# Optimization experiments

Measured on AMD Instinct MI355X. Metric: run time of the kernel, lower is better.

Reference implementation:

```python
import jax, jax.numpy as jnp
import numpy as np

# Dimensions
B, T_ENC, T_DEC = 64, 128, 64          # batch, encoder frames, max_video_length
DH, DV, CHUNK = 1024, 2048, 8          # dim_hidden, dim_video, ON-LSTM chunk size
NCH = DV // CHUNK                      # number of chunks (256)
G = 4 * DV + 2 * NCH                   # gate width of ON-LSTM cell


def setup_inputs() -> dict:
    key = jax.random.key(0)
    ks = jax.random.split(key, 6)
    s = lambda n: 1.0 / np.sqrt(n)
    return {
        "encoder_outputs": jax.random.normal(ks[0], (B, T_ENC, DH), jnp.float32),
        "encoder_hidden": jnp.zeros((1, B, DH), jnp.float32),  # unused by forward
        # Attention_update params: score over concat(enc_feat, query)
        "W_att1": (jax.random.normal(ks[1], (DH + DV, DH), jnp.float32) * s(DH + DV)),
        "b_att1": jnp.zeros((DH,), jnp.float32),
        "w_att2": (jax.random.normal(ks[2], (DH,), jnp.float32) * s(DH)),
        # ON-LSTM cell params (single layer: input DH -> hidden DV)
        "W_ih": (jax.random.normal(ks[3], (DH, G), jnp.float32) * s(DH)),
        "b_ih": jnp.zeros((G,), jnp.float32),
        "W_hh": (jax.random.normal(ks[4], (DV, G), jnp.float32) * s(DV)),
        "b_hh": jnp.zeros((G,), jnp.float32),
    }


def cumsoftmax(x):
    return jnp.cumsum(jax.nn.softmax(x, axis=-1), axis=-1)


def _decode(encoder_outputs, W_att1, b_att1, w_att2, W_ih, b_ih, W_hh, b_hh):
    b = encoder_outputs.shape[0]
    t_enc = encoder_outputs.shape[1]
    h0 = jnp.zeros((b, DV), encoder_outputs.dtype)
    c0 = jnp.zeros((b, NCH, CHUNK), encoder_outputs.dtype)

    def step(carry, _):
        h, c = carry
        # --- attention: additive score over encoder outputs, query = hidden ---
        q = jnp.broadcast_to(h[:, None, :], (b, t_enc, DV))
        feat = jnp.concatenate([encoder_outputs, q], axis=-1)        # (B,T,DH+DV)
        e = jnp.tanh(feat @ W_att1 + b_att1) @ w_att2                # (B,T)
        alpha = jax.nn.softmax(e, axis=-1)
        context = jnp.einsum("bt,btd->bd", alpha, encoder_outputs)  # (B,DH)
        # --- ON-LSTM cell ---
        gates = context @ W_ih + b_ih + h @ W_hh + b_hh              # (B,G)
        cingate = 1.0 - cumsoftmax(gates[:, :NCH])                   # master input gate
        cforgetgate = cumsoftmax(gates[:, NCH:2 * NCH])              # master forget gate
        r = gates[:, 2 * NCH:].reshape(b, 4 * NCH, CHUNK)
        o = jax.nn.sigmoid(r[:, :NCH])
        g = jnp.tanh(r[:, NCH:2 * NCH])
        i = jax.nn.sigmoid(r[:, 2 * NCH:3 * NCH])
        f = jax.nn.sigmoid(r[:, 3 * NCH:])
        cin = cingate[:, :, None]
        cfg = cforgetgate[:, :, None]
        overlap = cfg * cin
        fgate = f * overlap + (cfg - overlap)
        igate = i * overlap + (cin - overlap)
        cy = fgate * c + igate * g                                   # (B,NCH,CHUNK)
        hy = (o * jnp.tanh(cy)).reshape(b, DV)
        return (hy, cy), hy

    (_, _), outs = jax.lax.scan(step, (h0, c0), None, length=T_DEC)
    return jnp.transpose(outs, (1, 0, 2))  # (B, T_DEC, DV)


def reference(encoder_outputs, encoder_hidden, W_att1, b_att1, w_att2, W_ih, b_ih, W_hh, b_hh):
    return _decode(encoder_outputs, W_att1, b_att1, w_att2, W_ih, b_ih, W_hh, b_hh)
```

## Files before the change

### kernel.cpp

```cpp
#include <hip/hip_runtime.h>
#include <math.h>

#define BB   64
#define TENC 128
#define TDEC 64
#define DHH  1024
#define DVV  2048
#define NCHN 256
#define GG   8704

__device__ __forceinline__ float sigmoidf_(float x) { return 1.f / (1.f + expf(-x)); }

__global__ __launch_bounds__(256) void k_init(float* __restrict__ h, float* __restrict__ c) {
    int i = blockIdx.x * 256 + threadIdx.x;
    h[i] = 0.f;
    c[i] = 0.f;
}

__global__ __launch_bounds__(256) void k_P(const float* __restrict__ enc,
                                           const float* __restrict__ W1,
                                           const float* __restrict__ b1,
                                           float* __restrict__ P) {
    __shared__ float As[32][68];
    __shared__ float Bs[32][68];
    int j0 = blockIdx.x * 64;
    int m0 = blockIdx.y * 64;
    int tid = threadIdx.x;
    int jg = tid & 15, bg = tid >> 4;
    float acc[4][4] = {};
    for (int k0 = 0; k0 < DHH; k0 += 32) {
#pragma unroll
        for (int p = 0; p < 8; ++p) {
            int r = p * 8 + (tid >> 5);
            int kk = tid & 31;
            As[kk][r] = enc[(size_t)(m0 + r) * DHH + k0 + kk];
        }
#pragma unroll
        for (int p = 0; p < 8; ++p) {
            int kk = p * 4 + (tid >> 6);
            int jl = tid & 63;
            Bs[kk][jl] = W1[(size_t)(k0 + kk) * DHH + j0 + jl];
        }
        __syncthreads();
#pragma unroll
        for (int kk = 0; kk < 32; ++kk) {
            float4 a = *(const float4*)&As[kk][bg * 4];
            float4 b = *(const float4*)&Bs[kk][jg * 4];
            float av[4] = {a.x, a.y, a.z, a.w};
            float bv[4] = {b.x, b.y, b.z, b.w};
#pragma unroll
            for (int i = 0; i < 4; ++i)
#pragma unroll
                for (int j = 0; j < 4; ++j) acc[i][j] += av[i] * bv[j];
        }
        __syncthreads();
    }
    float4 bb = *(const float4*)&b1[j0 + jg * 4];
    float bia[4] = {bb.x, bb.y, bb.z, bb.w};
#pragma unroll
    for (int i = 0; i < 4; ++i) {
        int r = m0 + bg * 4 + i;
        float4 v = make_float4(acc[i][0] + bia[0], acc[i][1] + bia[1],
                               acc[i][2] + bia[2], acc[i][3] + bia[3]);
        *(float4*)&P[(size_t)r * DHH + j0 + jg * 4] = v;
    }
}

template <int KS>
__global__ __launch_bounds__(256) void k_skinny(const float* __restrict__ A1,
                                                const float* __restrict__ A2,
                                                const float* __restrict__ B1,
                                                const float* __restrict__ B2,
                                                int K1, int K2, int N,
                                                float* __restrict__ part) {
    __shared__ float As[32][68];
    __shared__ float Bs[32][68];
    int j0 = blockIdx.x * 64;
    int kseg = blockIdx.y;
    int tid = threadIdx.x;
    int jg = tid & 15, bg = tid >> 4;
    float acc[4][4] = {};
    for (int k0 = kseg * KS; k0 < (kseg + 1) * KS; k0 += 32) {
#pragma unroll
        for (int p = 0; p < 8; ++p) {
            int r = p * 8 + (tid >> 5);
            int kk = tid & 31;
            int k = k0 + kk;
            As[kk][r] = (k < K1) ? A1[r * K1 + k] : A2[r * K2 + (k - K1)];
        }
#pragma unroll
        for (int p = 0; p < 8; ++p) {
            int kk = p * 4 + (tid >> 6);
            int jl = tid & 63;
            int k = k0 + kk;
            Bs[kk][jl] = (k < K1) ? B1[(size_t)k * N + j0 + jl]
                                  : B2[(size_t)(k - K1) * N + j0 + jl];
        }
        __syncthreads();
#pragma unroll
        for (int kk = 0; kk < 32; ++kk) {
            float4 a = *(const float4*)&As[kk][bg * 4];
            float4 b = *(const float4*)&Bs[kk][jg * 4];
            float av[4] = {a.x, a.y, a.z, a.w};
            float bv[4] = {b.x, b.y, b.z, b.w};
#pragma unroll
            for (int i = 0; i < 4; ++i)
#pragma unroll
                for (int j = 0; j < 4; ++j) acc[i][j] += av[i] * bv[j];
        }
        __syncthreads();
    }
#pragma unroll
    for (int i = 0; i < 4; ++i) {
        int r = bg * 4 + i;
        float4 v = make_float4(acc[i][0], acc[i][1], acc[i][2], acc[i][3]);
        *(float4*)&part[(size_t)(kseg * 64 + r) * N + j0 + jg * 4] = v;
    }
}

__global__ __launch_bounds__(256) void k_e(const float* __restrict__ P,
                                           const float* __restrict__ hWp,
                                           const float* __restrict__ w2,
                                           float* __restrict__ e) {
    int b = blockIdx.x, tg = blockIdx.y;
    __shared__ float hw[DHH];
    __shared__ float w2s[DHH];
    int tid = threadIdx.x;
#pragma unroll
    for (int p = 0; p < 4; ++p) {
        int d = p * 256 + tid;
        float s = 0.f;
#pragma unroll
        for (int ks = 0; ks < 8; ++ks) s += hWp[(ks * 64 + b) * DHH + d];
        hw[d] = s;
        w2s[d] = w2[d];
    }
    __syncthreads();
    int wave = tid >> 6, lane = tid & 63;
    const float* Pb = P + (size_t)b * TENC * DHH;
    for (int tt = 0; tt < 8; ++tt) {
        int t = tg * 32 + wave * 8 + tt;
        const float* Pr = Pb + (size_t)t * DHH;
        float s = 0.f;
#pragma unroll
        for (int i = 0; i < 16; ++i) {
            int d = i * 64 + lane;
            s += tanhf(Pr[d] + hw[d]) * w2s[d];
        }
#pragma unroll
        for (int off = 32; off > 0; off >>= 1) s += __shfl_down(s, off);
        if (lane == 0) e[b * TENC + t] = s;
    }
}

__global__ __launch_bounds__(256) void k_sc(const float* __restrict__ e,
                                            const float* __restrict__ enc,
                                            float* __restrict__ ctx) {
    int b = blockIdx.x, dg = blockIdx.y;
    __shared__ float al[TENC];
    __shared__ float red[256];
    int tid = threadIdx.x;
    float v = (tid < TENC) ? e[b * TENC + tid] : -3.0e38f;
    red[tid] = v;
    __syncthreads();
    for (int s = 128; s > 0; s >>= 1) {
        if (tid < s) red[tid] = fmaxf(red[tid], red[tid + s]);
        __syncthreads();
    }
    float mx = red[0];
    __syncthreads();
    float ex = (tid < TENC) ? expf(v - mx) : 0.f;
    red[tid] = ex;
    __syncthreads();
    for (int s = 128; s > 0; s >>= 1) {
        if (tid < s) red[tid] += red[tid + s];
        __syncthreads();
    }
    float inv = 1.f / red[0];
    if (tid < TENC) al[tid] = ex * inv;
    __syncthreads();
    int d = dg * 256 + tid;
    const float* ep = enc + (size_t)b * TENC * DHH + d;
    float acc = 0.f;
#pragma unroll 4
    for (int t = 0; t < TENC; ++t) acc += al[t] * ep[(size_t)t * DHH];
    ctx[b * DHH + d] = acc;
}

__global__ __launch_bounds__(256) void k_pw(const float* __restrict__ part,
                                            const float* __restrict__ bih,
                                            const float* __restrict__ bhh,
                                            float* __restrict__ h,
                                            float* __restrict__ c,
                                            float* __restrict__ out, int t) {
    int b = blockIdx.x;
    __shared__ float g[GG];
    __shared__ float cs1[NCHN], cs2[NCHN], t1[NCHN], t2[NCHN];
    int tid = threadIdx.x;
    for (int p = 0; p < 34; ++p) {
        int j = p * 256 + tid;
        float s = bih[j] + bhh[j];
#pragma unroll
        for (int ks = 0; ks < 6; ++ks) s += part[(size_t)(ks * 64 + b) * GG + j];
        g[j] = s;
    }
    __syncthreads();
    float x1 = g[tid], x2 = g[NCHN + tid];
    t1[tid] = x1; t2[tid] = x2;
    __syncthreads();
    for (int s = 128; s > 0; s >>= 1) {
        if (tid < s) { t1[tid] = fmaxf(t1[tid], t1[tid + s]); t2[tid] = fmaxf(t2[tid], t2[tid + s]); }
        __syncthreads();
    }
    float m1 = t1[0], m2 = t2[0];
    __syncthreads();
    float e1 = expf(x1 - m1), e2 = expf(x2 - m2);
    t1[tid] = e1; t2[tid] = e2;
    __syncthreads();
    for (int s = 128; s > 0; s >>= 1) {
        if (tid < s) { t1[tid] += t1[tid + s]; t2[tid] += t2[tid + s]; }
        __syncthreads();
    }
    float inv1 = 1.f / t1[0], inv2 = 1.f / t2[0];
    __syncthreads();
    cs1[tid] = e1; cs2[tid] = e2;
    __syncthreads();
    for (int off = 1; off < NCHN; off <<= 1) {
        float a1 = (tid >= off) ? cs1[tid - off] : 0.f;
        float a2 = (tid >= off) ? cs2[tid - off] : 0.f;
        __syncthreads();
        cs1[tid] += a1; cs2[tid] += a2;
        __syncthreads();
    }
    float* cb = c + (size_t)b * DVV;
    float* hb = h + (size_t)b * DVV;
    float* ob = out + ((size_t)b * TDEC + t) * DVV;
    for (int p = 0; p < 8; ++p) {
        int idx = p * 256 + tid;
        int ch = idx >> 3;
        float cin = 1.f - cs1[ch] * inv1;
        float cfg = cs2[ch] * inv2;
        float ov = cfg * cin;
        float oo = sigmoidf_(g[512 + idx]);
        float gg = tanhf(g[2560 + idx]);
        float ii = sigmoidf_(g[4608 + idx]);
        float ff = sigmoidf_(g[6656 + idx]);
        float fg = ff * ov + (cfg - ov);
        float ig = ii * ov + (cin - ov);
        float cy = fg * cb[idx] + ig * gg;
        cb[idx] = cy;
        float hy = oo * tanhf(cy);
        hb[idx] = hy;
        ob[idx] = hy;
    }
}

extern "C" void kernel_launch(void* const* d_in, const int* in_sizes, int n_in,
                              void* d_out, int out_size, void* d_ws, size_t ws_size,
                              hipStream_t stream) {
    const float* enc    = (const float*)d_in[0];
    const float* W_att1 = (const float*)d_in[2];
    const float* b_att1 = (const float*)d_in[3];
    const float* w_att2 = (const float*)d_in[4];
    const float* W_ih   = (const float*)d_in[5];
    const float* b_ih   = (const float*)d_in[6];
    const float* W_hh   = (const float*)d_in[7];
    const float* b_hh   = (const float*)d_in[8];
    float* out = (float*)d_out;
    float* ws  = (float*)d_ws;

    float* P    = ws;
    float* hWp  = P + 8388608;
    float* ebuf = hWp + 524288;
    float* ctx  = ebuf + 8192;
    float* gp   = ctx + 65536;
    float* h    = gp + 3342336;
    float* c    = h + 131072;
    if (ws_size < 12591104ull * 4ull) return;

    k_init<<<512, 256, 0, stream>>>(h, c);
    k_P<<<dim3(16, 128), 256, 0, stream>>>(enc, W_att1, b_att1, P);

    const float* Wh_att = W_att1 + 1024 * 1024;
    for (int t = 0; t < TDEC; ++t) {
        k_skinny<256><<<dim3(16, 8), 256, 0, stream>>>(h, h, Wh_att, Wh_att,
                                                       2048, 2048, DHH, hWp);
        k_e<<<dim3(BB, 4), 256, 0, stream>>>(P, hWp, w_att2, ebuf);
        k_sc<<<dim3(BB, 4), 256, 0, stream>>>(ebuf, enc, ctx);
        k_skinny<512><<<dim3(136, 6), 256, 0, stream>>>(ctx, h, W_ih, W_hh,
                                                        1024, 2048, GG, gp);
        k_pw<<<BB, 256, 0, stream>>>(gp, b_ih, b_hh, h, c, out, t);
    }
}
```

Before: 10.04 ms.

## Use split-bf16 MFMA for recurrent GEMMs with pre-transposed converted weights

Converts the LSTM weights (W_ih/W_hh) into transposed hi/lo bf16 pairs once per call and the attention query weight into transposed bf16. The per-step skinny GEMMs now run on MFMA 16x16x32 bf16 instructions, using a three-product hi/lo split for the gate GEMM to keep near-fp32 accuracy and plain bf16 for the attention projection. The context and hidden state are written directly into packed bf16 activation buffers. This replaces the scalar fp32 FMA GEMMs but adds a one-time weight conversion, a much larger workspace requirement, and reduced precision in the attention-query path.

```diff
diff --git a/kernel.cpp b/kernel.cpp
--- a/kernel.cpp
+++ b/kernel.cpp
@@ -8,14 +8,20 @@
 #define DVV  2048
 #define NCHN 256
 #define GG   8704
+#define KTOT 3072
+
+typedef unsigned short u16;
+typedef __bf16 bf16x8 __attribute__((ext_vector_type(8)));
+typedef float  f32x4  __attribute__((ext_vector_type(4)));
 
 __device__ __forceinline__ float sigmoidf_(float x) { return 1.f / (1.f + expf(-x)); }
-
-__global__ __launch_bounds__(256) void k_init(float* __restrict__ h, float* __restrict__ c) {
-    int i = blockIdx.x * 256 + threadIdx.x;
-    h[i] = 0.f;
-    c[i] = 0.f;
-}
+__device__ __forceinline__ u16 f2bf(float f) {
+    unsigned u = __float_as_uint(f);
+    unsigned r = (u + 0x7fffu + ((u >> 16) & 1u)) >> 16;
+    return (u16)r;
+}
+__device__ __forceinline__ float bf2f(u16 s) { return __uint_as_float(((unsigned)s) << 16); }
+
 
 __global__ __launch_bounds__(256) void k_P(const float* __restrict__ enc,
                                            const float* __restrict__ W1,
@@ -64,6 +70,269 @@
                                acc[i][2] + bia[2], acc[i][3] + bia[3]);
         *(float4*)&P[(size_t)r * DHH + j0 + jg * 4] = v;
     }
+}
+
+__global__ __launch_bounds__(256) void k_e(const float* __restrict__ P,
+                                           const float* __restrict__ hWp,
+                                           const float* __restrict__ w2,
+                                           float* __restrict__ e) {
+    int b = blockIdx.x, tg = blockIdx.y;
+    __shared__ float hw[DHH];
+    __shared__ float w2s[DHH];
+    int tid = threadIdx.x;
+#pragma unroll
+    for (int p = 0; p < 4; ++p) {
+        int d = p * 256 + tid;
+        float s = 0.f;
+#pragma unroll
+        for (int ks = 0; ks < 8; ++ks) s += hWp[(ks * 64 + b) * DHH + d];
+        hw[d] = s;
+        w2s[d] = w2[d];
+    }
+    __syncthreads();
+    int wave = tid >> 6, lane = tid & 63;
+    const float* Pb = P + (size_t)b * TENC * DHH;
+    for (int tt = 0; tt < 8; ++tt) {
+        int t = tg * 32 + wave * 8 + tt;
+        const float* Pr = Pb + (size_t)t * DHH;
+        float s = 0.f;
+#pragma unroll
+        for (int i = 0; i < 16; ++i) {
+            int d = i * 64 + lane;
+            s += tanhf(Pr[d] + hw[d]) * w2s[d];
+        }
+#pragma unroll
+        for (int off = 32; off > 0; off >>= 1) s += __shfl_down(s, off);
+        if (lane == 0) e[b * TENC + t] = s;
+    }
+}
+
+
+__global__ __launch_bounds__(256) void k_init2(float* __restrict__ c,
+                                               u16* __restrict__ xh,
+                                               u16* __restrict__ xl) {
+    int i = blockIdx.x * 256 + threadIdx.x;
+    xh[i] = 0; xl[i] = 0;
+    if (i < BB * DVV) c[i] = 0.f;
+}
+
+template <bool LO>
+__global__ __launch_bounds__(256) void k_cvt(const float* __restrict__ S1,
+                                             const float* __restrict__ S2,
+                                             int K1, int N, int K,
+                                             u16* __restrict__ Dh,
+                                             u16* __restrict__ Dl) {
+    __shared__ float t[64][65];
+    int n0 = blockIdx.x * 64, k0 = blockIdx.y * 64;
+    int tid = threadIdx.x;
+    int cn = tid & 63, r4 = tid >> 6;
+#pragma unroll
+    for (int p = 0; p < 16; ++p) {
+        int kk = p * 4 + r4;
+        int kg = k0 + kk;
+        const float* src = (kg < K1) ? S1 + (size_t)kg * N : S2 + (size_t)(kg - K1) * N;
+        t[kk][cn] = src[n0 + cn];
+    }
+    __syncthreads();
+    int ck = tid & 63, n4 = tid >> 6;
+#pragma unroll
+    for (int p = 0; p < 16; ++p) {
+        int nn = p * 4 + n4;
+        float w = t[ck][nn];
+        u16 hi = f2bf(w);
+        size_t o = (size_t)(n0 + nn) * K + k0 + ck;
+        Dh[o] = hi;
+        if (LO) Dl[o] = f2bf(w - bf2f(hi));
+    }
+}
+
+__global__ __launch_bounds__(256) void k_mma1(const u16* __restrict__ xh,
+                                              const u16* __restrict__ Wta,
+                                              float* __restrict__ hWp) {
+    int n0 = blockIdx.x * 64;
+    int kseg = blockIdx.y;
+    int wv = threadIdx.x >> 6, l = threadIdx.x & 63;
+    int lr = l & 15, lk = (l >> 4) * 8;
+    int n = n0 + wv * 16 + lr;
+    const u16* wp = Wta + (size_t)n * 2048 + lk;
+    const u16* ap = xh + (size_t)lr * KTOT + 1024 + lk;
+    f32x4 z = {0.f, 0.f, 0.f, 0.f};
+    f32x4 acc[4];
+#pragma unroll
+    for (int mf = 0; mf < 4; ++mf) acc[mf] = z;
+    int kend = kseg * 256 + 256;
+    for (int k = kseg * 256; k < kend; k += 32) {
+        bf16x8 bfrag = *(const bf16x8*)(wp + k);
+#pragma unroll
+        for (int mf = 0; mf < 4; ++mf) {
+            bf16x8 a = *(const bf16x8*)(ap + (size_t)mf * 16 * KTOT + k);
+            acc[mf] = __builtin_amdgcn_mfma_f32_16x16x32_bf16(a, bfrag, acc[mf], 0, 0, 0);
+        }
+    }
+    float* dst = hWp + (size_t)kseg * 64 * DHH;
+#pragma unroll
+    for (int mf = 0; mf < 4; ++mf)
+#pragma unroll
+        for (int r = 0; r < 4; ++r) {
+            int m = mf * 16 + (l >> 4) * 4 + r;
+            dst[(size_t)m * DHH + n] = acc[mf][r];
+        }
+}
+
+__global__ __launch_bounds__(256) void k_mma3(const u16* __restrict__ xh,
+                                              const u16* __restrict__ xl,
+                                              const u16* __restrict__ Wh,
+                                              const u16* __restrict__ Wl,
+                                              float* __restrict__ part) {
+    int n0 = blockIdx.x * 64;
+    int kseg = blockIdx.y;
+    int wv = threadIdx.x >> 6, l = threadIdx.x & 63;
+    int lr = l & 15, lk = (l >> 4) * 8;
+    int n = n0 + wv * 16 + lr;
+    const u16* wph = Wh + (size_t)n * KTOT + lk;
+    const u16* wpl = Wl + (size_t)n * KTOT + lk;
+    const u16* aph = xh + (size_t)lr * KTOT + lk;
+    const u16* apl = xl + (size_t)lr * KTOT + lk;
+    f32x4 z = {0.f, 0.f, 0.f, 0.f};
+    f32x4 acc[4];
+#pragma unroll
+    for (int mf = 0; mf < 4; ++mf) acc[mf] = z;
+    int kend = kseg * 1536 + 1536;
+    for (int k = kseg * 1536; k < kend; k += 32) {
+        bf16x8 bh = *(const bf16x8*)(wph + k);
+        bf16x8 bl = *(const bf16x8*)(wpl + k);
+#pragma unroll
+        for (int mf = 0; mf < 4; ++mf) {
+            size_t ao = (size_t)mf * 16 * KTOT + k;
+            bf16x8 ah = *(const bf16x8*)(aph + ao);
+            bf16x8 al = *(const bf16x8*)(apl + ao);
+            acc[mf] = __builtin_amdgcn_mfma_f32_16x16x32_bf16(ah, bh, acc[mf], 0, 0, 0);
+            acc[mf] = __builtin_amdgcn_mfma_f32_16x16x32_bf16(ah, bl, acc[mf], 0, 0, 0);
+            acc[mf] = __builtin_amdgcn_mfma_f32_16x16x32_bf16(al, bh, acc[mf], 0, 0, 0);
+        }
+    }
+    float* dst = part + (size_t)kseg * 64 * GG;
+#pragma unroll
+    for (int mf = 0; mf < 4; ++mf)
+#pragma unroll
+        for (int r = 0; r < 4; ++r) {
+            int m = mf * 16 + (l >> 4) * 4 + r;
+            dst[(size_t)m * GG + n] = acc[mf][r];
+        }
+}
+
+__global__ __launch_bounds__(256) void k_sc2(const float* __restrict__ e,
+                                             const float* __restrict__ enc,
+                                             u16* __restrict__ xh,
+                                             u16* __restrict__ xl) {
+    int b = blockIdx.x, dg = blockIdx.y;
+    __shared__ float al[TENC];
+    __shared__ float red[256];
+    int tid = threadIdx.x;
+    float v = (tid < TENC) ? e[b * TENC + tid] : -3.0e38f;
+    red[tid] = v;
+    __syncthreads();
+    for (int s = 128; s > 0; s >>= 1) {
+        if (tid < s) red[tid] = fmaxf(red[tid], red[tid + s]);
+        __syncthreads();
+    }
+    float mx = red[0];
+    __syncthreads();
+    float ex = (tid < TENC) ? expf(v - mx) : 0.f;
+    red[tid] = ex;
+    __syncthreads();
+    for (int s = 128; s > 0; s >>= 1) {
+        if (tid < s) red[tid] += red[tid + s];
+        __syncthreads();
+    }
+    float inv = 1.f / red[0];
+    if (tid < TENC) al[tid] = ex * inv;
+    __syncthreads();
+    int d = dg * 256 + tid;
+    const float* ep = enc + (size_t)b * TENC * DHH + d;
+    float acc = 0.f;
+#pragma unroll 4
+    for (int t = 0; t < TENC; ++t) acc += al[t] * ep[(size_t)t * DHH];
+    u16 hi = f2bf(acc);
+    xh[(size_t)b * KTOT + d] = hi;
+    xl[(size_t)b * KTOT + d] = f2bf(acc - bf2f(hi));
+}
+
+__global__ __launch_bounds__(256) void k_pw2(const float* __restrict__ part,
+                                             const float* __restrict__ bih,
+                                             const float* __restrict__ bhh,
+                                             u16* __restrict__ xh,
+                                             u16* __restrict__ xl,
+                                             float* __restrict__ c,
+                                             float* __restrict__ out, int t) {
+    int b = blockIdx.x;
+    __shared__ float g[GG];
+    __shared__ float cs1[NCHN], cs2[NCHN], t1[NCHN], t2[NCHN];
+    int tid = threadIdx.x;
+    for (int p = 0; p < 34; ++p) {
+        int j = p * 256 + tid;
+        float s = bih[j] + bhh[j] + part[(size_t)b * GG + j] + part[(size_t)(64 + b) * GG + j];
+        g[j] = s;
+    }
+    __syncthreads();
+    float x1 = g[tid], x2 = g[NCHN + tid];
+    t1[tid] = x1; t2[tid] = x2;
+    __syncthreads();
+    for (int s = 128; s > 0; s >>= 1) {
+        if (tid < s) { t1[tid] = fmaxf(t1[tid], t1[tid + s]); t2[tid] = fmaxf(t2[tid], t2[tid + s]); }
+        __syncthreads();
+    }
+    float m1 = t1[0], m2 = t2[0];
+    __syncthreads();
+    float e1 = expf(x1 - m1), e2 = expf(x2 - m2);
+    t1[tid] = e1; t2[tid] = e2;
+    __syncthreads();
+    for (int s = 128; s > 0; s >>= 1) {
+        if (tid < s) { t1[tid] += t1[tid + s]; t2[tid] += t2[tid + s]; }
+        __syncthreads();
+    }
+    float inv1 = 1.f / t1[0], inv2 = 1.f / t2[0];
+    __syncthreads();
+    cs1[tid] = e1; cs2[tid] = e2;
+    __syncthreads();
+    for (int off = 1; off < NCHN; off <<= 1) {
+        float a1 = (tid >= off) ? cs1[tid - off] : 0.f;
+        float a2 = (tid >= off) ? cs2[tid - off] : 0.f;
+        __syncthreads();
+        cs1[tid] += a1; cs2[tid] += a2;
+        __syncthreads();
+    }
+    float* cb = c + (size_t)b * DVV;
+    float* ob = out + ((size_t)b * TDEC + t) * DVV;
+    u16* xhb = xh + (size_t)b * KTOT + 1024;
+    u16* xlb = xl + (size_t)b * KTOT + 1024;
+    for (int p = 0; p < 8; ++p) {
+        int idx = p * 256 + tid;
+        int ch = idx >> 3;
+        float cin = 1.f - cs1[ch] * inv1;
+        float cfg = cs2[ch] * inv2;
+        float ov = cfg * cin;
+        float oo = sigmoidf_(g[512 + idx]);
+        float gg = tanhf(g[2560 + idx]);
+        float ii = sigmoidf_(g[4608 + idx]);
+        float ff = sigmoidf_(g[6656 + idx]);
+        float fg = ff * ov + (cfg - ov);
+        float ig = ii * ov + (cin - ov);
+        float cy = fg * cb[idx] + ig * gg;
+        cb[idx] = cy;
+        float hy = oo * tanhf(cy);
+        ob[idx] = hy;
+        u16 hh = f2bf(hy);
+        xhb[idx] = hh;
+        xlb[idx] = f2bf(hy - bf2f(hh));
+    }
+}
+
+
+__global__ __launch_bounds__(256) void k_init(float* __restrict__ h, float* __restrict__ c) {
+    int i = blockIdx.x * 256 + threadIdx.x;
+    h[i] = 0.f;
+    c[i] = 0.f;
 }
 
 template <int KS>
@@ -118,44 +387,9 @@
     }
 }
 
-__global__ __launch_bounds__(256) void k_e(const float* __restrict__ P,
-                                           const float* __restrict__ hWp,
-                                           const float* __restrict__ w2,
-                                           float* __restrict__ e) {
-    int b = blockIdx.x, tg = blockIdx.y;
-    __shared__ float hw[DHH];
-    __shared__ float w2s[DHH];
-    int tid = threadIdx.x;
-#pragma unroll
-    for (int p = 0; p < 4; ++p) {
-        int d = p * 256 + tid;
-        float s = 0.f;
-#pragma unroll
-        for (int ks = 0; ks < 8; ++ks) s += hWp[(ks * 64 + b) * DHH + d];
-        hw[d] = s;
-        w2s[d] = w2[d];
-    }
-    __syncthreads();
-    int wave = tid >> 6, lane = tid & 63;
-    const float* Pb = P + (size_t)b * TENC * DHH;
-    for (int tt = 0; tt < 8; ++tt) {
-        int t = tg * 32 + wave * 8 + tt;
-        const float* Pr = Pb + (size_t)t * DHH;
-        float s = 0.f;
-#pragma unroll
-        for (int i = 0; i < 16; ++i) {
-            int d = i * 64 + lane;
-            s += tanhf(Pr[d] + hw[d]) * w2s[d];
-        }
-#pragma unroll
-        for (int off = 32; off > 0; off >>= 1) s += __shfl_down(s, off);
-        if (lane == 0) e[b * TENC + t] = s;
-    }
-}
-
-__global__ __launch_bounds__(256) void k_sc(const float* __restrict__ e,
-                                            const float* __restrict__ enc,
-                                            float* __restrict__ ctx) {
+__global__ __launch_bounds__(256) void k_sc_f32(const float* __restrict__ e,
+                                                const float* __restrict__ enc,
+                                                float* __restrict__ ctx) {
     int b = blockIdx.x, dg = blockIdx.y;
     __shared__ float al[TENC];
     __shared__ float red[256];
@@ -187,12 +421,12 @@
     ctx[b * DHH + d] = acc;
 }
 
-__global__ __launch_bounds__(256) void k_pw(const float* __restrict__ part,
-                                            const float* __restrict__ bih,
-                                            const float* __restrict__ bhh,
-                                            float* __restrict__ h,
-                                            float* __restrict__ c,
-                                            float* __restrict__ out, int t) {
+__global__ __launch_bounds__(256) void k_pw_f32(const float* __restrict__ part,
+                                                const float* __restrict__ bih,
+                                                const float* __restrict__ bhh,
+                                                float* __restrict__ h,
+                                                float* __restrict__ c,
+                                                float* __restrict__ out, int t) {
     int b = blockIdx.x;
     __shared__ float g[GG];
     __shared__ float cs1[NCHN], cs2[NCHN], t1[NCHN], t2[NCHN];
@@ -255,6 +489,7 @@
     }
 }
 
+
 extern "C" void kernel_launch(void* const* d_in, const int* in_sizes, int n_in,
                               void* d_out, int out_size, void* d_ws, size_t ws_size,
                               hipStream_t stream) {
@@ -269,26 +504,52 @@
     float* out = (float*)d_out;
     float* ws  = (float*)d_ws;
 
-    float* P    = ws;
-    float* hWp  = P + 8388608;
-    float* ebuf = hWp + 524288;
-    float* ctx  = ebuf + 8192;
-    float* gp   = ctx + 65536;
-    float* h    = gp + 3342336;
-    float* c    = h + 131072;
-    if (ws_size < 12591104ull * 4ull) return;
-
-    k_init<<<512, 256, 0, stream>>>(h, c);
-    k_P<<<dim3(16, 128), 256, 0, stream>>>(enc, W_att1, b_att1, P);
-
-    const float* Wh_att = W_att1 + 1024 * 1024;
-    for (int t = 0; t < TDEC; ++t) {
-        k_skinny<256><<<dim3(16, 8), 256, 0, stream>>>(h, h, Wh_att, Wh_att,
-                                                       2048, 2048, DHH, hWp);
-        k_e<<<dim3(BB, 4), 256, 0, stream>>>(P, hWp, w_att2, ebuf);
-        k_sc<<<dim3(BB, 4), 256, 0, stream>>>(ebuf, enc, ctx);
-        k_skinny<512><<<dim3(136, 6), 256, 0, stream>>>(ctx, h, W_ih, W_hh,
-                                                        1024, 2048, GG, gp);
-        k_pw<<<BB, 256, 0, stream>>>(gp, b_ih, b_hh, h, c, out, t);
-    }
-}
+    if (ws_size >= 152600576ull) {
+        float* P    = ws;
+        float* hWp  = P + 8388608;
+        float* ebuf = hWp + 524288;
+        float* gp   = ebuf + 8192;
+        float* c    = gp + 1114112;
+        u16* xh  = (u16*)(c + 131072);
+        u16* xl  = xh + 196608;
+        u16* Wth = xl + 196608;
+        u16* Wtl = Wth + 26738688;
+        u16* Wta = Wtl + 26738688;
+
+        k_init2<<<768, 256, 0, stream>>>(c, xh, xl);
+        k_cvt<true><<<dim3(136, 48), 256, 0, stream>>>(W_ih, W_hh, 1024, GG, KTOT, Wth, Wtl);
+        const float* Wh_att = W_att1 + 1024 * 1024;
+        k_cvt<false><<<dim3(16, 32), 256, 0, stream>>>(Wh_att, Wh_att, 2048, DHH, 2048, Wta, Wta);
+        k_P<<<dim3(16, 128), 256, 0, stream>>>(enc, W_att1, b_att1, P);
+
+        for (int t = 0; t < TDEC; ++t) {
+            k_mma1<<<dim3(16, 8), 256, 0, stream>>>(xh, Wta, hWp);
+            k_e<<<dim3(BB, 4), 256, 0, stream>>>(P, hWp, w_att2, ebuf);
+            k_sc2<<<dim3(BB, 4), 256, 0, stream>>>(ebuf, enc, xh, xl);
+            k_mma3<<<dim3(136, 2), 256, 0, stream>>>(xh, xl, Wth, Wtl, gp);
+            k_pw2<<<BB, 256, 0, stream>>>(gp, b_ih, b_hh, xh, xl, c, out, t);
+        }
+    } else if (ws_size >= 12591104ull * 4ull) {
+        float* P    = ws;
+        float* hWp  = P + 8388608;
+        float* ebuf = hWp + 524288;
+        float* ctx  = ebuf + 8192;
+        float* gp   = ctx + 65536;
+        float* h    = gp + 3342336;
+        float* c    = h + 131072;
+
+        k_init<<<512, 256, 0, stream>>>(h, c);
+        k_P<<<dim3(16, 128), 256, 0, stream>>>(enc, W_att1, b_att1, P);
+
+        const float* Wh_att = W_att1 + 1024 * 1024;
+        for (int t = 0; t < TDEC; ++t) {
+            k_skinny<256><<<dim3(16, 8), 256, 0, stream>>>(h, h, Wh_att, Wh_att,
+                                                           2048, 2048, DHH, hWp);
+            k_e<<<dim3(BB, 4), 256, 0, stream>>>(P, hWp, w_att2, ebuf);
+            k_sc_f32<<<dim3(BB, 4), 256, 0, stream>>>(ebuf, enc, ctx);
+            k_skinny<512><<<dim3(136, 6), 256, 0, stream>>>(ctx, h, W_ih, W_hh,
+                                                            1024, 2048, GG, gp);
+            k_pw_f32<<<BB, 256, 0, stream>>>(gp, b_ih, b_hh, h, c, out, t);
+        }
+    }
+}
```

Measured after the change: 12.10 ms. 20.5% more time.
